# Performance work log

Hardware: AMD Instinct MI355X
Metric: run time of the kernel (lower is better)

The kernel has to match this reference:

```python
import jax, jax.numpy as jnp
import numpy as np

FORE_TH = 0.5
BACK_TH = 0.4
MAX_FOR_TARGET = True
FOREGROUND_ONLY = False  # return both foreground and background masks


def _cxcywh_to_xyxy(b):
    cx, cy, w, h = b[..., 0], b[..., 1], b[..., 2], b[..., 3]
    return jnp.stack([cx - w * 0.5, cy - h * 0.5, cx + w * 0.5, cy + h * 0.5], axis=-1)


def _batch_iou(anchors_xyxy, boxes_xyxy):
    # anchors_xyxy: [A,4], boxes_xyxy: [B,T,4] -> ious [B,A,T]
    a = anchors_xyxy[None, :, None, :]   # [1,A,1,4]
    b = boxes_xyxy[:, None, :, :]        # [B,1,T,4]
    lt = jnp.maximum(a[..., :2], b[..., :2])
    rb = jnp.minimum(a[..., 2:], b[..., 2:])
    wh = jnp.clip(rb - lt, 0.0)
    inter = wh[..., 0] * wh[..., 1]                                   # [B,A,T]
    area_a = (a[..., 2] - a[..., 0]) * (a[..., 3] - a[..., 1])
    area_b = (b[..., 2] - b[..., 0]) * (b[..., 3] - b[..., 1])
    return inter / (area_a + area_b - inter + 1e-9)


def setup_inputs() -> dict:
    key = jax.random.key(0)
    k1, k2 = jax.random.split(key)
    labels = jax.random.uniform(k1, (8, 64, 84), dtype=jnp.float32)
    anchors = jax.random.uniform(k2, (1, 100000, 4), dtype=jnp.float32)
    return {"labels": labels, "anchors": anchors}


def reference(labels, anchors):
    # labels: [B, T, 4+C] (cxcywh + class), anchors: [1, A, 4] (cxcywh)
    B = labels.shape[0]
    a_xyxy = _cxcywh_to_xyxy(anchors[0])           # [A,4]
    b_xyxy = _cxcywh_to_xyxy(labels[..., :4])      # [B,T,4]
    ious = _batch_iou(a_xyxy, b_xyxy)              # [B,A,T]

    max_iou_anchor = jnp.max(ious, axis=2)         # [B,A] best IoU per anchor
    target_for_anchor = jnp.argmax(ious, axis=2)   # [B,A] best target per anchor

    fore_mask = max_iou_anchor >= FORE_TH          # [B,A]
    if MAX_FOR_TARGET:
        anchor_for_target = jnp.argmax(ious, axis=1)        # [B,T] best anchor per target
        batch_idx = jnp.arange(B)[:, None]
        fm_t = jnp.zeros(fore_mask.shape, dtype=bool).at[batch_idx, anchor_for_target].set(True)
        fore_mask = jnp.logical_or(fore_mask, fm_t)

    back_mask = jnp.logical_not(fore_mask)
    if BACK_TH is not None:
        back_mask = jnp.logical_and(back_mask, max_iou_anchor < BACK_TH)

    # label[target_for_anchor] per batch -> [B, A, 4+C]
    assigned_target = jnp.take_along_axis(labels, target_for_anchor[..., None], axis=1)

    # Fixed-shape equivalent of the original list-of-dicts with nonzero():
    # (foreground mask, background mask, per-anchor assigned labels).
    return fore_mask, back_mask, assigned_target
```

## Files before the change

kernel.cpp:

```cpp
#include <hip/hip_runtime.h>
#include <stdint.h>

#define N_ANCH 100000
#define BATCH 8
#define NTGT 64
#define NFEAT 84
#define BLK_A 256
#define NBX ((N_ANCH + BLK_A - 1) / BLK_A)

__global__ __launch_bounds__(BLK_A) void assign_kernel(
    const float* __restrict__ labels,
    const float* __restrict__ anchors,
    float* __restrict__ out_fore,
    float* __restrict__ out_back,
    int* __restrict__ ws_tgt,
    unsigned long long* __restrict__ ws_part)
{
#pragma clang fp contract(off)
    __shared__ float sbx1[NTGT], sby1[NTGT], sbx2[NTGT], sby2[NTGT], sarea[NTGT];
    __shared__ unsigned long long sbest[NTGT];

    const int b   = blockIdx.y;
    const int tid = threadIdx.x;

    if (tid < NTGT) {
        const float4 box = *(const float4*)(labels + ((size_t)b * NTGT + tid) * NFEAT);
        const float x1 = box.x - box.z * 0.5f;
        const float y1 = box.y - box.w * 0.5f;
        const float x2 = box.x + box.z * 0.5f;
        const float y2 = box.y + box.w * 0.5f;
        sbx1[tid] = x1; sby1[tid] = y1; sbx2[tid] = x2; sby2[tid] = y2;
        sarea[tid] = (x2 - x1) * (y2 - y1);
        sbest[tid] = 0ull;
    }
    __syncthreads();

    const int n = blockIdx.x * BLK_A + tid;
    if (n < N_ANCH) {
        const float4 ab = *(const float4*)(anchors + (size_t)n * 4);
        const float ax1 = ab.x - ab.z * 0.5f;
        const float ay1 = ab.y - ab.w * 0.5f;
        const float ax2 = ab.x + ab.z * 0.5f;
        const float ay2 = ab.y + ab.w * 0.5f;
        const float areaA = (ax2 - ax1) * (ay2 - ay1);

        const unsigned long long pn =
            (unsigned long long)(0xFFFFFFFFu - (uint32_t)n);

        unsigned long long bestA = 0ull;
        for (int s = 0; s < NTGT; ++s) {
            const int t = (tid + s) & (NTGT - 1);
            const float ltx = fmaxf(ax1, sbx1[t]);
            const float lty = fmaxf(ay1, sby1[t]);
            const float rbx = fminf(ax2, sbx2[t]);
            const float rby = fminf(ay2, sby2[t]);
            const float w = fmaxf(rbx - ltx, 0.0f);
            const float h = fmaxf(rby - lty, 0.0f);
            const float inter = w * h;
            const float denom = ((areaA + sarea[t]) - inter) + 1e-9f;
            const float iou = inter / denom;
            const uint32_t ib = __float_as_uint(iou);

            const unsigned long long pa =
                ((unsigned long long)ib << 6) | (unsigned long long)(63 - t);
            bestA = pa > bestA ? pa : bestA;

            atomicMax(&sbest[t], ((unsigned long long)ib << 32) | pn);
        }

        const float maxIou = __uint_as_float((uint32_t)(bestA >> 6));
        const int   bt     = 63 - (int)(bestA & 63u);
        const bool fore = (maxIou >= 0.5f);
        const bool back = (!fore) && (maxIou < 0.4f);
        const size_t o = (size_t)b * N_ANCH + n;
        out_fore[o] = fore ? 1.0f : 0.0f;
        out_back[o] = back ? 1.0f : 0.0f;
        ws_tgt[o] = bt;
    }
    __syncthreads();

    if (tid < NTGT) {
        ws_part[((size_t)b * NBX + blockIdx.x) * NTGT + tid] = sbest[tid];
    }
}

__global__ __launch_bounds__(256) void fixup_kernel(
    const unsigned long long* __restrict__ ws_part,
    float* __restrict__ out_fore,
    float* __restrict__ out_back)
{
    const int tid = blockIdx.x * blockDim.x + threadIdx.x;
    if (tid >= BATCH * NTGT) return;
    const int b = tid >> 6;
    const int t = tid & 63;
    unsigned long long best = 0ull;
    for (int blk = 0; blk < NBX; ++blk) {
        const unsigned long long v = ws_part[((size_t)b * NBX + blk) * NTGT + t];
        best = v > best ? v : best;
    }
    const uint32_t n = 0xFFFFFFFFu - (uint32_t)(best & 0xFFFFFFFFull);
    const size_t o = (size_t)b * N_ANCH + n;
    out_fore[o] = 1.0f;
    out_back[o] = 0.0f;
}

#define GATHER_CHUNKS (NFEAT / 4)
__global__ __launch_bounds__(256) void gather_kernel(
    const float* __restrict__ labels,
    const int* __restrict__ ws_tgt,
    float* __restrict__ out_assigned)
{
    const int b = blockIdx.y;
    const int idx = blockIdx.x * 256 + threadIdx.x;
    if (idx >= N_ANCH * GATHER_CHUNKS) return;
    const int n = idx / GATHER_CHUNKS;
    const int k = idx - n * GATHER_CHUNKS;
    const int tgt = ws_tgt[(size_t)b * N_ANCH + n];
    const float4 v = *(const float4*)(labels + ((size_t)b * NTGT + tgt) * NFEAT + k * 4);
    *(float4*)(out_assigned + ((size_t)b * N_ANCH + n) * NFEAT + (size_t)k * 4) = v;
}

extern "C" void kernel_launch(void* const* d_in, const int* in_sizes, int n_in,
                              void* d_out, int out_size, void* d_ws, size_t ws_size,
                              hipStream_t stream) {
    const float* labels  = (const float*)d_in[0];
    const float* anchors = (const float*)d_in[1];

    float* out_fore     = (float*)d_out;
    float* out_back     = out_fore + (size_t)BATCH * N_ANCH;
    float* out_assigned = out_back + (size_t)BATCH * N_ANCH;

    int* ws_tgt = (int*)d_ws;
    size_t tgt_bytes = ((size_t)BATCH * N_ANCH * sizeof(int) + 255) & ~(size_t)255;
    unsigned long long* ws_part = (unsigned long long*)((char*)d_ws + tgt_bytes);

    dim3 gridA(NBX, BATCH);
    assign_kernel<<<gridA, BLK_A, 0, stream>>>(labels, anchors, out_fore, out_back,
                                               ws_tgt, ws_part);

    fixup_kernel<<<2, 256, 0, stream>>>(ws_part, out_fore, out_back);

    const int nchunks = N_ANCH * GATHER_CHUNKS;
    dim3 gridC((nchunks + 255) / 256, BATCH);
    gather_kernel<<<gridC, 256, 0, stream>>>(labels, ws_tgt, out_assigned);
}
```

Baseline: 349.1 us.

## Fuse gather into assign kernel and parallelize per-target fixup reduction

Moves the label gather into the assignment kernel, using a shared-memory index array so the per-anchor target indices no longer round-trip through a global workspace and one launch is dropped. Splits the per-target shared atomicMax board per wave to reduce contention, and packs target boxes into float4 in shared memory. The fixup becomes one 64-lane block per (batch,target) with a shuffle reduction over a transposed partials layout, replacing a 512-thread serial scan over about 391 blocks. The fused kernel does more work per block, and target areas are now recomputed inside the inner loop.

Measured after the change: 293.1 us. 1.19x faster.

```diff
diff --git a/kernel.cpp b/kernel.cpp
--- a/kernel.cpp
+++ b/kernel.cpp
@@ -6,36 +6,37 @@
 #define NTGT 64
 #define NFEAT 84
 #define BLK_A 256
+#define NWAVE (BLK_A / 64)
 #define NBX ((N_ANCH + BLK_A - 1) / BLK_A)
+#define GCHUNK (NFEAT / 4)
 
-__global__ __launch_bounds__(BLK_A) void assign_kernel(
+__global__ __launch_bounds__(BLK_A) void fused_kernel(
     const float* __restrict__ labels,
     const float* __restrict__ anchors,
     float* __restrict__ out_fore,
     float* __restrict__ out_back,
-    int* __restrict__ ws_tgt,
+    float* __restrict__ out_assigned,
     unsigned long long* __restrict__ ws_part)
 {
 #pragma clang fp contract(off)
-    __shared__ float sbx1[NTGT], sby1[NTGT], sbx2[NTGT], sby2[NTGT], sarea[NTGT];
-    __shared__ unsigned long long sbest[NTGT];
+    __shared__ float4 tbox[NTGT];
+    __shared__ unsigned long long sbest[NWAVE * NTGT];
+    __shared__ int sidx[BLK_A];
 
-    const int b   = blockIdx.y;
-    const int tid = threadIdx.x;
+    const int b    = blockIdx.y;
+    const int bx   = blockIdx.x;
+    const int tid  = threadIdx.x;
+    const int wave = tid >> 6;
 
     if (tid < NTGT) {
         const float4 box = *(const float4*)(labels + ((size_t)b * NTGT + tid) * NFEAT);
-        const float x1 = box.x - box.z * 0.5f;
-        const float y1 = box.y - box.w * 0.5f;
-        const float x2 = box.x + box.z * 0.5f;
-        const float y2 = box.y + box.w * 0.5f;
-        sbx1[tid] = x1; sby1[tid] = y1; sbx2[tid] = x2; sby2[tid] = y2;
-        sarea[tid] = (x2 - x1) * (y2 - y1);
-        sbest[tid] = 0ull;
+        tbox[tid] = make_float4(box.x - box.z * 0.5f, box.y - box.w * 0.5f,
+                                box.x + box.z * 0.5f, box.y + box.w * 0.5f);
     }
+    sbest[tid] = 0ull;
     __syncthreads();
 
-    const int n = blockIdx.x * BLK_A + tid;
+    const int n = bx * BLK_A + tid;
     if (n < N_ANCH) {
         const float4 ab = *(const float4*)(anchors + (size_t)n * 4);
         const float ax1 = ab.x - ab.z * 0.5f;
@@ -46,18 +47,21 @@
 
         const unsigned long long pn =
             (unsigned long long)(0xFFFFFFFFu - (uint32_t)n);
+        unsigned long long bestA = 0ull;
+        unsigned long long* myboard = sbest + wave * NTGT;
 
-        unsigned long long bestA = 0ull;
         for (int s = 0; s < NTGT; ++s) {
             const int t = (tid + s) & (NTGT - 1);
-            const float ltx = fmaxf(ax1, sbx1[t]);
-            const float lty = fmaxf(ay1, sby1[t]);
-            const float rbx = fminf(ax2, sbx2[t]);
-            const float rby = fminf(ay2, sby2[t]);
+            const float4 tb = tbox[t];
+            const float areaB = (tb.z - tb.x) * (tb.w - tb.y);
+            const float ltx = fmaxf(ax1, tb.x);
+            const float lty = fmaxf(ay1, tb.y);
+            const float rbx = fminf(ax2, tb.z);
+            const float rby = fminf(ay2, tb.w);
             const float w = fmaxf(rbx - ltx, 0.0f);
             const float h = fmaxf(rby - lty, 0.0f);
             const float inter = w * h;
-            const float denom = ((areaA + sarea[t]) - inter) + 1e-9f;
+            const float denom = ((areaA + areaB) - inter) + 1e-9f;
             const float iou = inter / denom;
             const uint32_t ib = __float_as_uint(iou);
 
@@ -65,7 +69,7 @@
                 ((unsigned long long)ib << 6) | (unsigned long long)(63 - t);
             bestA = pa > bestA ? pa : bestA;
 
-            atomicMax(&sbest[t], ((unsigned long long)ib << 32) | pn);
+            atomicMax(&myboard[t], ((unsigned long long)ib << 32) | pn);
         }
 
         const float maxIou = __uint_as_float((uint32_t)(bestA >> 6));
@@ -75,49 +79,60 @@
         const size_t o = (size_t)b * N_ANCH + n;
         out_fore[o] = fore ? 1.0f : 0.0f;
         out_back[o] = back ? 1.0f : 0.0f;
-        ws_tgt[o] = bt;
+        sidx[tid] = bt;
+    } else {
+        sidx[tid] = 0;
     }
     __syncthreads();
 
     if (tid < NTGT) {
-        ws_part[((size_t)b * NBX + blockIdx.x) * NTGT + tid] = sbest[tid];
+        unsigned long long m0 = sbest[tid];
+        unsigned long long m1 = sbest[NTGT + tid];
+        unsigned long long m2 = sbest[2 * NTGT + tid];
+        unsigned long long m3 = sbest[3 * NTGT + tid];
+        unsigned long long a = m0 > m1 ? m0 : m1;
+        unsigned long long c = m2 > m3 ? m2 : m3;
+        ws_part[((size_t)b * NTGT + tid) * NBX + bx] = a > c ? a : c;
+    }
+
+    const float* lab_b = labels + (size_t)b * NTGT * NFEAT;
+    float* out_b = out_assigned + ((size_t)b * N_ANCH + (size_t)bx * BLK_A) * NFEAT;
+    for (int i = tid; i < BLK_A * GCHUNK; i += BLK_A) {
+        const int nl = i / GCHUNK;
+        const int k  = i - nl * GCHUNK;
+        if (bx * BLK_A + nl < N_ANCH) {
+            const int t = sidx[nl];
+            const float4 v = *(const float4*)(lab_b + (size_t)t * NFEAT + k * 4);
+            *(float4*)(out_b + (size_t)nl * NFEAT + (size_t)k * 4) = v;
+        }
     }
 }
 
-__global__ __launch_bounds__(256) void fixup_kernel(
+__global__ __launch_bounds__(64) void fixup_kernel(
     const unsigned long long* __restrict__ ws_part,
     float* __restrict__ out_fore,
     float* __restrict__ out_back)
 {
-    const int tid = blockIdx.x * blockDim.x + threadIdx.x;
-    if (tid >= BATCH * NTGT) return;
-    const int b = tid >> 6;
-    const int t = tid & 63;
+    const int bt   = blockIdx.x;
+    const int lane = threadIdx.x;
+    const unsigned long long* p = ws_part + (size_t)bt * NBX;
+
     unsigned long long best = 0ull;
-    for (int blk = 0; blk < NBX; ++blk) {
-        const unsigned long long v = ws_part[((size_t)b * NBX + blk) * NTGT + t];
+    for (int i = lane; i < NBX; i += 64) {
+        const unsigned long long v = p[i];
         best = v > best ? v : best;
     }
-    const uint32_t n = 0xFFFFFFFFu - (uint32_t)(best & 0xFFFFFFFFull);
-    const size_t o = (size_t)b * N_ANCH + n;
-    out_fore[o] = 1.0f;
-    out_back[o] = 0.0f;
-}
-
-#define GATHER_CHUNKS (NFEAT / 4)
-__global__ __launch_bounds__(256) void gather_kernel(
-    const float* __restrict__ labels,
-    const int* __restrict__ ws_tgt,
-    float* __restrict__ out_assigned)
-{
-    const int b = blockIdx.y;
-    const int idx = blockIdx.x * 256 + threadIdx.x;
-    if (idx >= N_ANCH * GATHER_CHUNKS) return;
-    const int n = idx / GATHER_CHUNKS;
-    const int k = idx - n * GATHER_CHUNKS;
-    const int tgt = ws_tgt[(size_t)b * N_ANCH + n];
-    const float4 v = *(const float4*)(labels + ((size_t)b * NTGT + tgt) * NFEAT + k * 4);
-    *(float4*)(out_assigned + ((size_t)b * N_ANCH + n) * NFEAT + (size_t)k * 4) = v;
+    for (int off = 32; off > 0; off >>= 1) {
+        const unsigned long long o = __shfl_down(best, off, 64);
+        best = o > best ? o : best;
+    }
+    if (lane == 0) {
+        const uint32_t n = 0xFFFFFFFFu - (uint32_t)(best & 0xFFFFFFFFull);
+        const int b = bt >> 6;
+        const size_t o = (size_t)b * N_ANCH + n;
+        out_fore[o] = 1.0f;
+        out_back[o] = 0.0f;
+    }
 }
 
 extern "C" void kernel_launch(void* const* d_in, const int* in_sizes, int n_in,
@@ -130,17 +145,11 @@
     float* out_back     = out_fore + (size_t)BATCH * N_ANCH;
     float* out_assigned = out_back + (size_t)BATCH * N_ANCH;
 
-    int* ws_tgt = (int*)d_ws;
-    size_t tgt_bytes = ((size_t)BATCH * N_ANCH * sizeof(int) + 255) & ~(size_t)255;
-    unsigned long long* ws_part = (unsigned long long*)((char*)d_ws + tgt_bytes);
+    unsigned long long* ws_part = (unsigned long long*)d_ws;
 
     dim3 gridA(NBX, BATCH);
-    assign_kernel<<<gridA, BLK_A, 0, stream>>>(labels, anchors, out_fore, out_back,
-                                               ws_tgt, ws_part);
+    fused_kernel<<<gridA, BLK_A, 0, stream>>>(labels, anchors, out_fore, out_back,
+                                              out_assigned, ws_part);
 
-    fixup_kernel<<<2, 256, 0, stream>>>(ws_part, out_fore, out_back);
-
-    const int nchunks = N_ANCH * GATHER_CHUNKS;
-    dim3 gridC((nchunks + 255) / 256, BATCH);
-    gather_kernel<<<gridC, 256, 0, stream>>>(labels, ws_tgt, out_assigned);
+    fixup_kernel<<<BATCH * NTGT, 64, 0, stream>>>(ws_part, out_fore, out_back);
 }
```
